# Performance work log

Measured on AMD Instinct MI355X. Metric: run time of the kernel, lower is better.

## Reference

```python
import jax, jax.numpy as jnp
import numpy as np

D_MODEL = 1024
NUM_HEADS = 16
D_FF = 4096
MAX_SEQ_LEN = 2048
THETA = 10000.0
EPS = 1e-5
B, S = 2, 2048


def setup_inputs() -> dict:
    key = jax.random.key(0)
    ks = jax.random.split(key, 10)
    scale = 0.02
    inp = {
        "in_features": jax.random.normal(ks[0], (B, S, D_MODEL), dtype=jnp.float32),
        "token_positions": jnp.broadcast_to(jnp.arange(S, dtype=jnp.int32), (B, S)),
        "q_w": jax.random.normal(ks[1], (D_MODEL, D_MODEL), dtype=jnp.float32) * scale,
        "k_w": jax.random.normal(ks[2], (D_MODEL, D_MODEL), dtype=jnp.float32) * scale,
        "v_w": jax.random.normal(ks[3], (D_MODEL, D_MODEL), dtype=jnp.float32) * scale,
        "o_w": jax.random.normal(ks[4], (D_MODEL, D_MODEL), dtype=jnp.float32) * scale,
        "ln1_w": jnp.ones((D_MODEL,), dtype=jnp.float32),
        "ln2_w": jnp.ones((D_MODEL,), dtype=jnp.float32),
        "ffn_w1": jax.random.normal(ks[5], (D_FF, D_MODEL), dtype=jnp.float32) * scale,
        "ffn_w2": jax.random.normal(ks[6], (D_MODEL, D_FF), dtype=jnp.float32) * scale,
        "ffn_w3": jax.random.normal(ks[7], (D_FF, D_MODEL), dtype=jnp.float32) * scale,
    }
    return inp


def _rmsnorm(x, w, eps=EPS):
    return x * jax.lax.rsqrt(jnp.mean(x * x, axis=-1, keepdims=True) + eps) * w


def _rope(x, pos, theta=THETA):
    # x: [B, H, S, Dh]; pos: [B, S] int
    dh = x.shape[-1]
    inv_freq = theta ** (-jnp.arange(0, dh, 2, dtype=jnp.float32) / dh)  # [Dh/2]
    ang = pos.astype(jnp.float32)[..., None] * inv_freq                  # [B, S, Dh/2]
    cos = jnp.cos(ang)[:, None, :, :]  # [B, 1, S, Dh/2]
    sin = jnp.sin(ang)[:, None, :, :]
    x1, x2 = x[..., 0::2], x[..., 1::2]
    r1 = x1 * cos - x2 * sin
    r2 = x1 * sin + x2 * cos
    return jnp.stack([r1, r2], axis=-1).reshape(x.shape)


def _block(x, pos, q_w, k_w, v_w, o_w, ln1_w, ln2_w, w1, w2, w3):
    b, s, d = x.shape
    h, dh = NUM_HEADS, d // NUM_HEADS
    # Pre-LN attention
    xn = _rmsnorm(x, ln1_w)
    q = jnp.einsum('bsd,ed->bse', xn, q_w).reshape(b, s, h, dh).transpose(0, 2, 1, 3)
    k = jnp.einsum('bsd,ed->bse', xn, k_w).reshape(b, s, h, dh).transpose(0, 2, 1, 3)
    v = jnp.einsum('bsd,ed->bse', xn, v_w).reshape(b, s, h, dh).transpose(0, 2, 1, 3)
    q = _rope(q, pos)
    k = _rope(k, pos)
    scores = jnp.einsum('bhqd,bhkd->bhqk', q, k) / jnp.sqrt(jnp.float32(dh))
    causal = jnp.tril(jnp.ones((s, s), dtype=bool))
    scores = jnp.where(causal, scores, jnp.float32(-1e9))
    attn = jax.nn.softmax(scores, axis=-1)
    ctx = jnp.einsum('bhqk,bhkd->bhqd', attn, v).transpose(0, 2, 1, 3).reshape(b, s, d)
    attn_out = jnp.einsum('bsd,ed->bse', ctx, o_w)
    x = x + attn_out
    # Pre-LN SwiGLU FFN
    xn2 = _rmsnorm(x, ln2_w)
    g = jnp.einsum('bsd,fd->bsf', xn2, w1)
    u = jnp.einsum('bsd,fd->bsf', xn2, w3)
    ffn_out = jnp.einsum('bsf,df->bsd', jax.nn.silu(g) * u, w2)
    return x + ffn_out


def reference(in_features, token_positions, q_w, k_w, v_w, o_w, ln1_w, ln2_w, ffn_w1, ffn_w2, ffn_w3):
    return _block(in_features, token_positions, q_w, k_w, v_w, o_w, ln1_w, ln2_w, ffn_w1, ffn_w2, ffn_w3)
```

## Files before the change

kernel.cpp:

```cpp
#include <hip/hip_runtime.h>
#include <hip/hip_bf16.h>

typedef __attribute__((ext_vector_type(8))) __bf16 bf16x8;
typedef __attribute__((ext_vector_type(4))) float f32x4;

#define DEV static __device__ __forceinline__

DEV unsigned short f2bf(float f) {
  __bf16 h = (__bf16)f;
  union { __bf16 h; unsigned short u; } v; v.h = h;
  return v.u;
}
DEV float bf2f(unsigned short h) {
  union { unsigned int u; float f; } v; v.u = ((unsigned int)h) << 16;
  return v.f;
}
DEV f32x4 mfma16(bf16x8 a, bf16x8 b, f32x4 c) {
  return __builtin_amdgcn_mfma_f32_16x16x32_bf16(a, b, c, 0, 0, 0);
}
DEV void gload_lds16(const void* g, void* l) {
  __builtin_amdgcn_global_load_lds((__attribute__((address_space(1))) void*)g,
                                   (__attribute__((address_space(3))) void*)l,
                                   16, 0, 0);
}
#if __has_builtin(__builtin_amdgcn_exp2f)
DEV float fexp2(float x) { return __builtin_amdgcn_exp2f(x); }
#else
DEV float fexp2(float x) { return exp2f(x); }
#endif

struct CvtArgs { const float* src[7]; int cum[8]; };
__global__ __launch_bounds__(256) void cvt_all(CvtArgs a, unsigned short* __restrict__ dst) {
  int i = (blockIdx.x * 256 + threadIdx.x) * 4;
  if (i >= a.cum[7]) return;
  int w = 0;
#pragma unroll 7
  for (int t = 0; t < 7; ++t) if (i >= a.cum[t + 1]) w = t + 1;
  float4 v = *(const float4*)(a.src[w] + (i - a.cum[w]));
  dst[i + 0] = f2bf(v.x);
  dst[i + 1] = f2bf(v.y);
  dst[i + 2] = f2bf(v.z);
  dst[i + 3] = f2bf(v.w);
}

__global__ __launch_bounds__(256) void rmsnorm_k(const float* __restrict__ x,
                                                 const float* __restrict__ w,
                                                 unsigned short* __restrict__ out) {
  int row = blockIdx.x;
  int tid = threadIdx.x;
  const float* xr = x + (size_t)row * 1024;
  float4 v = *(const float4*)(xr + tid * 4);
  float ss = v.x * v.x + v.y * v.y + v.z * v.z + v.w * v.w;
#pragma unroll
  for (int m = 32; m >= 1; m >>= 1) ss += __shfl_xor(ss, m);
  __shared__ float red[4];
  int wid = tid >> 6;
  if ((tid & 63) == 0) red[wid] = ss;
  __syncthreads();
  float tot = red[0] + red[1] + red[2] + red[3];
  float rs = rsqrtf(tot * (1.0f / 1024.0f) + 1e-5f);
  float4 wv = *(const float4*)(w + tid * 4);
  unsigned short* o = out + (size_t)row * 1024 + tid * 4;
  o[0] = f2bf(v.x * rs * wv.x);
  o[1] = f2bf(v.y * rs * wv.y);
  o[2] = f2bf(v.z * rs * wv.z);
  o[3] = f2bf(v.w * rs * wv.w);
}

__global__ __launch_bounds__(256) void rope2_k(unsigned short* __restrict__ q,
                                               unsigned short* __restrict__ k,
                                               const int* __restrict__ pos) {
  int gid = blockIdx.x * 256 + threadIdx.x;
  unsigned short* x = (gid < 2097152) ? q : k;
  int idx = gid & 2097151;
  int i = idx & 31;
  int s = (idx >> 5) & 2047;
  int bh = idx >> 16;
  int b = bh >> 4;
  float p = (float)pos[b * 2048 + s];
  float inv = exp2f(-(float)i * 0.4152410118609203f);
  float ang = p * inv;
  float sn = sinf(ang), cs = cosf(ang);
  size_t base = (((size_t)bh * 2048) + s) * 64 + 2 * i;
  float x1 = bf2f(x[base]), x2 = bf2f(x[base + 1]);
  x[base]     = f2bf(x1 * cs - x2 * sn);
  x[base + 1] = f2bf(x1 * sn + x2 * cs);
}

template <int MODE>
DEV void gemm8_body(const unsigned short* __restrict__ A, int lda,
                    const unsigned short* __restrict__ B, int ldb,
                    int bm, int bn, int kbase, int nt,
                    unsigned short* __restrict__ outb, float* __restrict__ outf,
                    const float* __restrict__ resid, const unsigned short* __restrict__ gate,
                    unsigned short* As, unsigned short* Bs) {
  const int tid = threadIdx.x;
  const int lane = tid & 63, wid = tid >> 6;
  const int wr = wid >> 2, wc = wid & 3;
  const int m0 = bm * 256, n0 = bn * 256;

  const int r0 = tid >> 2, r1 = 128 + (tid >> 2), cc = tid & 3;
  const int sc0 = (cc ^ ((r0 >> 1) & 3)) * 8;
  const int sc1 = (cc ^ ((r1 >> 1) & 3)) * 8;
  const size_t arow0 = (size_t)(m0 + r0) * lda, arow1 = (size_t)(m0 + r1) * lda;
  const size_t brow0 = (size_t)(n0 + r0) * ldb, brow1 = (size_t)(n0 + r1) * ldb;
  const int du0 = tid * 8, du1 = (512 + tid) * 8;

  auto stA = [&](int t, int kh) {
    unsigned short* d = As + ((((t & 1) << 1) | kh) * 8192);
    const unsigned short* s = A + kbase + t * 64 + kh * 32;
    gload_lds16(s + arow0 + sc0, d + du0);
    gload_lds16(s + arow1 + sc1, d + du1);
  };
  auto stB = [&](int t, int kh) {
    unsigned short* d = Bs + ((((t & 1) << 1) | kh) * 8192);
    const unsigned short* s = B + kbase + t * 64 + kh * 32;
    gload_lds16(s + brow0 + sc0, d + du0);
    gload_lds16(s + brow1 + sc1, d + du1);
  };

  const int fcol = ((lane >> 4) ^ ((lane >> 1) & 3)) * 8;
  const int frow = lane & 15;
  const int abase = (wr * 128 + frow) * 32 + fcol;
  const int bbase = (wc * 64 + frow) * 32 + fcol;

  f32x4 acc[8][4] = {};
  bf16x8 a[4], b[4];

#define LOADA(buf, ks, mh) { const unsigned short* p_ = As + (((buf) << 1) | (ks)) * 8192 + abase + (mh) * 2048; \
  a[0] = *(const bf16x8*)(p_); a[1] = *(const bf16x8*)(p_ + 512); \
  a[2] = *(const bf16x8*)(p_ + 1024); a[3] = *(const bf16x8*)(p_ + 1536); }
#define LOADB(buf, ks) { const unsigned short* p_ = Bs + (((buf) << 1) | (ks)) * 8192 + bbase; \
  b[0] = *(const bf16x8*)(p_); b[1] = *(const bf16x8*)(p_ + 512); \
  b[2] = *(const bf16x8*)(p_ + 1024); b[3] = *(const bf16x8*)(p_ + 1536); }
#define MFMAQ(mh) { _Pragma("unroll") for (int fi = 0; fi < 4; ++fi) \
  _Pragma("unroll") for (int j = 0; j < 4; ++j) \
    acc[(mh) * 4 + fi][j] = mfma16(a[fi], b[j], acc[(mh) * 4 + fi][j]); }
#define LGK0() { asm volatile("s_waitcnt lgkmcnt(0)" ::: "memory"); __builtin_amdgcn_sched_barrier(0); }

  stA(0, 0); stB(0, 0); stA(0, 1); stB(0, 1);
  stA(1, 0); stB(1, 0);
  asm volatile("s_waitcnt vmcnt(4)" ::: "memory");
  __builtin_amdgcn_s_barrier();

  for (int t = 0; t < nt; ++t) {
    const int buf = t & 1;
    LOADA(buf, 0, 0); LOADB(buf, 0);
    if (t + 1 < nt) stA(t + 1, 1);
    __builtin_amdgcn_s_barrier();
    LGK0();
    __builtin_amdgcn_s_setprio(1); MFMAQ(0); __builtin_amdgcn_s_setprio(0);
    __builtin_amdgcn_s_barrier();
    LOADA(buf, 0, 1);
    if (t + 1 < nt) stB(t + 1, 1);
    __builtin_amdgcn_s_barrier();
    LGK0();
    __builtin_amdgcn_s_setprio(1); MFMAQ(1); __builtin_amdgcn_s_setprio(0);
    __builtin_amdgcn_s_barrier();
    LOADA(buf, 1, 0); LOADB(buf, 1);
    if (t + 2 < nt) stA(t + 2, 0);
    __builtin_amdgcn_s_barrier();
    LGK0();
    __builtin_amdgcn_s_setprio(1); MFMAQ(0); __builtin_amdgcn_s_setprio(0);
    __builtin_amdgcn_s_barrier();
    LOADA(buf, 1, 1);
    if (t + 2 < nt) stB(t + 2, 0);
    __builtin_amdgcn_s_barrier();
    LGK0();
    __builtin_amdgcn_s_setprio(1); MFMAQ(1); __builtin_amdgcn_s_setprio(0);
    if (t + 1 < nt) {
      if (t + 2 < nt) { asm volatile("s_waitcnt vmcnt(4)" ::: "memory"); }
      else            { asm volatile("s_waitcnt vmcnt(0)" ::: "memory"); }
      __builtin_amdgcn_s_barrier();
    }
  }
#undef LOADA
#undef LOADB
#undef MFMAQ
#undef LGK0

#pragma unroll
  for (int i = 0; i < 8; ++i)
#pragma unroll
    for (int j = 0; j < 4; ++j)
#pragma unroll
      for (int r = 0; r < 4; ++r) {
        int m = m0 + wr * 128 + i * 16 + ((lane >> 4) << 2) + r;
        int n = n0 + wc * 64 + j * 16 + (lane & 15);
        float v = acc[i][j][r];
        if (MODE == 0) {
          unsigned short* dst = outb + ((n >= 1024) ? 4194304 : 0);
          int nn = n & 1023;
          int bb = m >> 11, s = m & 2047, hh = nn >> 6, dd = nn & 63;
          dst[(((size_t)bb * 16 + hh) * 2048 + s) * 64 + dd] = f2bf(v);
        } else if (MODE == 1) {
          int hh = m >> 6, dd = m & 63, bb = n >> 11, s = n & 2047;
          outb[(((size_t)bb * 16 + hh) * 64 + dd) * 2048 + s] = f2bf(v);
        } else if (MODE == 2) {
          size_t idx = (size_t)m * 1024 + n;
          outf[idx] = resid[idx] + v;
        } else if (MODE == 3) {
          outb[(size_t)m * 4096 + n] = f2bf(v);
        } else if (MODE == 4) {
          size_t idx = (size_t)m * 4096 + n;
          float g = bf2f(gate[idx]);
          outb[idx] = f2bf(g / (1.0f + __expf(-g)) * v);
        } else {
          outf[(size_t)m * 1024 + n] = v;
        }
      }
}

DEV void swz_map(int bid, int nwg, int MT, int& bm, int& bn) {
  int cpx = nwg >> 3;
  int sw = (bid & 7) * cpx + (bid >> 3);
  bm = sw % MT;
  bn = sw / MT;
}

template <int MODE>
__global__ __launch_bounds__(512, 2) void gemm8_k(const unsigned short* __restrict__ A, int lda,
                                                  const unsigned short* __restrict__ B, int ldb,
                                                  int MT, int kz, int nt,
                                                  unsigned short* __restrict__ outb,
                                                  float* __restrict__ outf,
                                                  const float* __restrict__ resid,
                                                  const unsigned short* __restrict__ gate) {
  __shared__ __align__(16) unsigned short lds[65536];
  int bm, bn;
  swz_map(blockIdx.x, gridDim.x, MT, bm, bn);
  int kb = kz * blockIdx.y;
  float* of = outf;
  if (MODE == 5) of += (size_t)blockIdx.y * 4194304;
  gemm8_body<MODE>(A, lda, B, ldb, bm, bn, kb, nt, outb, of, resid, gate, lds, lds + 32768);
}

__global__ __launch_bounds__(512, 2) void gemm8_qkv(const unsigned short* __restrict__ xn,
                                                    const unsigned short* __restrict__ wqk,
                                                    const unsigned short* __restrict__ wv,
                                                    unsigned short* __restrict__ qk_out,
                                                    unsigned short* __restrict__ vt_out) {
  __shared__ __align__(16) unsigned short lds[65536];
  int bid = blockIdx.x;
  if (bid < 128) {
    int bm, bn;
    swz_map(bid, 128, 16, bm, bn);
    gemm8_body<0>(xn, 1024, wqk, 1024, bm, bn, 0, 16, qk_out, nullptr, nullptr, nullptr, lds, lds + 32768);
  } else {
    bid -= 128;
    int bm, bn;
    swz_map(bid, 64, 4, bm, bn);
    gemm8_body<1>(wv, 1024, xn, 1024, bm, bn, 0, 16, vt_out, nullptr, nullptr, nullptr, lds, lds + 32768);
  }
}

__global__ __launch_bounds__(256) void gemm_wo(const unsigned short* __restrict__ A,
                                               const unsigned short* __restrict__ Bw,
                                               float* __restrict__ outf,
                                               const float* __restrict__ resid) {
  __shared__ __align__(16) unsigned short As[128 * 64];
  __shared__ __align__(16) unsigned short Bs[128 * 64];
  const int K = 1024, N = 1024;
  const int tid = threadIdx.x;
  const int wid = tid >> 6, lane = tid & 63;
  const int wr = wid >> 1, wc = wid & 1;
  const int m0 = blockIdx.x * 128, n0 = blockIdx.y * 128;
  const int sw = (lane & 7) * 8;
  f32x4 acc[4][4] = {};

  for (int k0 = 0; k0 < K; k0 += 64) {
    __syncthreads();
#pragma unroll
    for (int it = 0; it < 4; ++it) {
      int c = wid * 4 + it;
      int row = c * 8 + (lane >> 3);
      int col = ((lane & 7) ^ (row & 7)) * 8;
      gload_lds16(A + (size_t)(m0 + row) * K + k0 + col, As + c * 512);
      gload_lds16(Bw + (size_t)(n0 + row) * K + k0 + col, Bs + c * 512);
    }
    asm volatile("s_waitcnt vmcnt(0)" ::: "memory");
    __syncthreads();
#pragma unroll
    for (int kk = 0; kk < 2; ++kk) {
      const int kof = (kk * 32 + (lane >> 4) * 8) ^ sw;
      bf16x8 af[4], bfr[4];
#pragma unroll
      for (int i = 0; i < 4; ++i) {
        af[i]  = *(const bf16x8*)(As + (wr * 64 + i * 16 + (lane & 15)) * 64 + kof);
        bfr[i] = *(const bf16x8*)(Bs + (wc * 64 + i * 16 + (lane & 15)) * 64 + kof);
      }
#pragma unroll
      for (int i = 0; i < 4; ++i)
#pragma unroll
        for (int j = 0; j < 4; ++j) acc[i][j] = mfma16(af[i], bfr[j], acc[i][j]);
    }
  }
  const int rb = m0 + wr * 64 + ((lane >> 4) * 4);
  const int cb = n0 + wc * 64 + (lane & 15);
#pragma unroll
  for (int i = 0; i < 4; ++i)
#pragma unroll
    for (int r = 0; r < 4; ++r) {
      int m = rb + i * 16 + r;
#pragma unroll
      for (int j = 0; j < 4; ++j) {
        size_t idx = (size_t)m * N + cb + j * 16;
        outf[idx] = resid[idx] + acc[i][j][r];
      }
    }
}

__global__ __launch_bounds__(256) void reduce_k(float* __restrict__ out,
                                                const float* __restrict__ part) {
  int i = (blockIdx.x * 256 + threadIdx.x) * 4;
  float4 o = *(const float4*)(out + i);
  float4 p0 = *(const float4*)(part + i);
  float4 p1 = *(const float4*)(part + 4194304 + i);
  float4 p2 = *(const float4*)(part + 8388608 + i);
  float4 p3 = *(const float4*)(part + 12582912 + i);
  o.x += p0.x + p1.x + p2.x + p3.x;
  o.y += p0.y + p1.y + p2.y + p3.y;
  o.z += p0.z + p1.z + p2.z + p3.z;
  o.w += p0.w + p1.w + p2.w + p3.w;
  *(float4*)(out + i) = o;
}

__global__ __launch_bounds__(256) void attn_k(const unsigned short* __restrict__ q,
                                              const unsigned short* __restrict__ k,
                                              const unsigned short* __restrict__ vt,
                                              unsigned short* __restrict__ ctx) {
  __shared__ __align__(16) unsigned short Ks[2][64 * 64];
  __shared__ __align__(16) unsigned short Vs[2][64 * 64];
  __shared__ __align__(16) unsigned short Ps[4][16 * 64];
  const int bid = blockIdx.x;
  const int bh = (bid & 7) * 4 + ((bid >> 3) & 3);
  const int qt = 31 - (bid >> 5);
  const int tid = threadIdx.x, wid = tid >> 6, lane = tid & 63;
  const size_t bhS = (size_t)bh * 2048;
  const size_t bhD = (size_t)bh * 64 * 2048;
  const int b = bh >> 4, hh = bh & 15;
  const int sw = (lane & 7) * 8;
  const float SC2 = 0.18033688011112042f;

  const int c0 = wid * 2, c1 = wid * 2 + 1;
  const int row0 = c0 * 8 + (lane >> 3), row1 = c1 * 8 + (lane >> 3);
  const int col0 = ((lane & 7) ^ (row0 & 7)) * 8;
  const int col1 = ((lane & 7) ^ (row1 & 7)) * 8;

  auto stage = [&](int kt, int buf) {
    gload_lds16(k + (bhS + kt * 64 + row0) * 64 + col0, &Ks[buf][c0 * 512]);
    gload_lds16(k + (bhS + kt * 64 + row1) * 64 + col1, &Ks[buf][c1 * 512]);
    gload_lds16(vt + bhD + (size_t)row0 * 2048 + kt * 64 + col0, &Vs[buf][c0 * 512]);
    gload_lds16(vt + bhD + (size_t)row1 * 2048 + kt * 64 + col1, &Vs[buf][c1 * 512]);
  };

  const int q0 = qt * 64;
  bf16x8 qf[2];
  {
    const unsigned short* qp = q + (bhS + q0 + wid * 16 + (lane & 15)) * 64 + (lane >> 4) * 8;
    qf[0] = *(const bf16x8*)qp;
    qf[1] = *(const bf16x8*)(qp + 32);
#pragma unroll
    for (int jj = 0; jj < 8; ++jj) {
      qf[0][jj] = (__bf16)((float)qf[0][jj] * SC2);
      qf[1][jj] = (__bf16)((float)qf[1][jj] * SC2);
    }
  }
  float mrow[4], lrow[4];
  f32x4 o[4] = {};
#pragma unroll
  for (int r = 0; r < 4; ++r) { mrow[r] = -1e30f; lrow[r] = 0.0f; }
  const int rowb = q0 + wid * 16 + ((lane >> 4) * 4);

  stage(0, 0);
  if (qt > 0) { stage(1, 1); asm volatile("s_waitcnt vmcnt(4)" ::: "memory"); }
  else        {              asm volatile("s_waitcnt vmcnt(0)" ::: "memory"); }
  __builtin_amdgcn_s_barrier();

  for (int kt = 0; kt <= qt; ++kt) {
    const int cur = kt & 1;
    f32x4 s[4];
#pragma unroll
    for (int nt = 0; nt < 4; ++nt) {
      f32x4 z = {};
#pragma unroll
      for (int ks = 0; ks < 2; ++ks) {
        int kof = (ks * 32 + (lane >> 4) * 8) ^ sw;
        bf16x8 kf = *(const bf16x8*)(&Ks[cur][(nt * 16 + (lane & 15)) * 64 + kof]);
        z = mfma16(qf[ks], kf, z);
      }
      s[nt] = z;
    }
    const bool diag = (kt == qt);
    float pm[4];
    bool ok = true;
#pragma unroll
    for (int r = 0; r < 4; ++r) {
      float mx = -3e38f;
#pragma unroll
      for (int nt = 0; nt < 4; ++nt) {
        float val = s[nt][r];
        if (diag && (kt * 64 + nt * 16 + (lane & 15)) > (rowb + r)) val = -3e38f;
        s[nt][r] = val;
        mx = fmaxf(mx, val);
      }
      mx = fmaxf(mx, __shfl_xor(mx, 1));
      mx = fmaxf(mx, __shfl_xor(mx, 2));
      mx = fmaxf(mx, __shfl_xor(mx, 4));
      mx = fmaxf(mx, __shfl_xor(mx, 8));
      pm[r] = mx;
      ok = ok && (mx <= mrow[r] + 11.5f);
    }
    if (!__all(ok)) {
#pragma unroll
      for (int r = 0; r < 4; ++r) {
        float mn = fmaxf(mrow[r], pm[r]);
        float al = fexp2(mrow[r] - mn);
        lrow[r] *= al;
#pragma unroll
        for (int d = 0; d < 4; ++d) o[d][r] *= al;
        mrow[r] = mn;
      }
    }
#pragma unroll
    for (int r = 0; r < 4; ++r) {
      float sum = 0.0f;
#pragma unroll
      for (int nt = 0; nt < 4; ++nt) {
        float pv = fexp2(s[nt][r] - mrow[r]);
        s[nt][r] = pv;
        sum += pv;
      }
      lrow[r] += sum;
    }
#pragma unroll
    for (int nt = 0; nt < 4; ++nt)
#pragma unroll
      for (int r = 0; r < 4; ++r) {
        int qr = (lane >> 4) * 4 + r;
        Ps[wid][qr * 64 + ((nt * 16 + (lane & 15)) ^ ((qr & 7) * 8))] = f2bf(s[nt][r]);
      }
#pragma unroll
    for (int ks = 0; ks < 2; ++ks) {
      int qr2 = lane & 15;
      bf16x8 pf = *(const bf16x8*)(&Ps[wid][qr2 * 64 + ((ks * 32 + (lane >> 4) * 8) ^ ((qr2 & 7) * 8))]);
      int kof = (ks * 32 + (lane >> 4) * 8) ^ sw;
#pragma unroll
      for (int d = 0; d < 4; ++d) {
        bf16x8 vf = *(const bf16x8*)(&Vs[cur][(d * 16 + (lane & 15)) * 64 + kof]);
        o[d] = mfma16(pf, vf, o[d]);
      }
    }
    __builtin_amdgcn_s_barrier();
    if (kt + 2 <= qt) {
      stage(kt + 2, cur);
      asm volatile("s_waitcnt vmcnt(4)" ::: "memory");
    } else if (kt + 1 <= qt) {
      asm volatile("s_waitcnt vmcnt(0)" ::: "memory");
    }
    __builtin_amdgcn_s_barrier();
  }
#pragma unroll
  for (int r = 0; r < 4; ++r) {
    lrow[r] += __shfl_xor(lrow[r], 1);
    lrow[r] += __shfl_xor(lrow[r], 2);
    lrow[r] += __shfl_xor(lrow[r], 4);
    lrow[r] += __shfl_xor(lrow[r], 8);
  }
#pragma unroll
  for (int d = 0; d < 4; ++d)
#pragma unroll
    for (int r = 0; r < 4; ++r) {
      float val = o[d][r] / lrow[r];
      ctx[((size_t)b * 2048 + (rowb + r)) * 1024 + hh * 64 + d * 16 + (lane & 15)] = f2bf(val);
    }
}

extern "C" void kernel_launch(void* const* d_in, const int* in_sizes, int n_in,
                              void* d_out, int out_size, void* d_ws, size_t ws_size,
                              hipStream_t stream) {
  (void)in_sizes; (void)n_in; (void)out_size; (void)ws_size;
  const float* in_f = (const float*)d_in[0];
  const int* pos    = (const int*)d_in[1];
  const float* q_w  = (const float*)d_in[2];
  const float* k_w  = (const float*)d_in[3];
  const float* v_w  = (const float*)d_in[4];
  const float* o_w  = (const float*)d_in[5];
  const float* ln1  = (const float*)d_in[6];
  const float* ln2  = (const float*)d_in[7];
  const float* w1   = (const float*)d_in[8];
  const float* w2   = (const float*)d_in[9];
  const float* w3   = (const float*)d_in[10];
  float* out = (float*)d_out;

  unsigned short* ws = (unsigned short*)d_ws;
  unsigned short* wb   = ws;
  unsigned short* wqkb = wb;
  unsigned short* wvb  = wb + 2097152;
  unsigned short* wob  = wb + 3145728;
  unsigned short* w1b  = wb + 4194304;
  unsigned short* w2b  = wb + 8388608;
  unsigned short* w3b  = wb + 12582912;
  unsigned short* xn   = ws + 16777216;
  unsigned short* qb   = ws + 20971520;
  unsigned short* kb   = ws + 25165824;
  unsigned short* vb   = ws + 29360128;
  unsigned short* cx   = ws + 33554432;
  unsigned short* gb   = ws + 37748736;
  float* part          = (float*)(ws + 20971520);
  unsigned short* hb   = ws + 54525952;

  CvtArgs ca;
  ca.src[0] = q_w; ca.src[1] = k_w; ca.src[2] = v_w; ca.src[3] = o_w;
  ca.src[4] = w1;  ca.src[5] = w2;  ca.src[6] = w3;
  ca.cum[0] = 0;        ca.cum[1] = 1048576;  ca.cum[2] = 2097152;  ca.cum[3] = 3145728;
  ca.cum[4] = 4194304;  ca.cum[5] = 8388608;  ca.cum[6] = 12582912; ca.cum[7] = 16777216;
  cvt_all<<<16384, 256, 0, stream>>>(ca, wb);

  rmsnorm_k<<<4096, 256, 0, stream>>>(in_f, ln1, xn);

  gemm8_qkv<<<192, 512, 0, stream>>>(xn, wqkb, wvb, qb, vb);

  rope2_k<<<16384, 256, 0, stream>>>(qb, kb, pos);

  attn_k<<<1024, 256, 0, stream>>>(qb, kb, vb, cx);

  gemm_wo<<<dim3(32, 8), 256, 0, stream>>>(cx, wob, out, in_f);

  rmsnorm_k<<<4096, 256, 0, stream>>>(out, ln2, xn);

  gemm8_k<3><<<256, 512, 0, stream>>>(xn, 1024, w1b, 1024, 16, 0, 16, gb, nullptr, nullptr, nullptr);
  gemm8_k<4><<<256, 512, 0, stream>>>(xn, 1024, w3b, 1024, 16, 0, 16, hb, nullptr, nullptr, gb);
  gemm8_k<5><<<dim3(64, 4), 512, 0, stream>>>(hb, 4096, w2b, 4096, 16, 1024, 16, nullptr, part, nullptr, nullptr);

  reduce_k<<<4096, 256, 0, stream>>>(out, part);
}
```

Before: 294.4 us.

## Transpose attention scores, fuse rope q/k, fuse FFN down-proj with residual

The attention kernel now computes S^T (K as the A operand) so each lane owns one query row. Row max and sum then need only two cross-lane shuffles, and P is written to LDS as packed bf16 pairs with a padded stride instead of scalar swizzled stores. RoPE handles q and k in the same thread with half the grid. The split-K FFN down-projection plus separate reduce kernel is replaced by a templated 128x128 residual GEMM (K=4096) that adds into out directly. This removes the partial buffer traffic and one launch, but that GEMM loses the larger 256x256 tile and split-K parallelism. It also changes fexp2 to always use exp2f.

Measured after the change: 294.1 us. Within noise of the previous version (-0.1%).

```diff
diff --git a/kernel.cpp b/kernel.cpp
--- a/kernel.cpp
+++ b/kernel.cpp
@@ -15,6 +15,11 @@
   union { unsigned int u; float f; } v; v.u = ((unsigned int)h) << 16;
   return v.f;
 }
+DEV unsigned pkbf(float lo, float hi) {
+  union { __bf16 h[2]; unsigned u; } v;
+  v.h[0] = (__bf16)lo; v.h[1] = (__bf16)hi;
+  return v.u;
+}
 DEV f32x4 mfma16(bf16x8 a, bf16x8 b, f32x4 c) {
   return __builtin_amdgcn_mfma_f32_16x16x32_bf16(a, b, c, 0, 0, 0);
 }
@@ -23,11 +28,7 @@
                                    (__attribute__((address_space(3))) void*)l,
                                    16, 0, 0);
 }
-#if __has_builtin(__builtin_amdgcn_exp2f)
-DEV float fexp2(float x) { return __builtin_amdgcn_exp2f(x); }
-#else
 DEV float fexp2(float x) { return exp2f(x); }
-#endif
 
 struct CvtArgs { const float* src[7]; int cum[8]; };
 __global__ __launch_bounds__(256) void cvt_all(CvtArgs a, unsigned short* __restrict__ dst) {
@@ -70,9 +71,7 @@
 __global__ __launch_bounds__(256) void rope2_k(unsigned short* __restrict__ q,
                                                unsigned short* __restrict__ k,
                                                const int* __restrict__ pos) {
-  int gid = blockIdx.x * 256 + threadIdx.x;
-  unsigned short* x = (gid < 2097152) ? q : k;
-  int idx = gid & 2097151;
+  int idx = blockIdx.x * 256 + threadIdx.x;
   int i = idx & 31;
   int s = (idx >> 5) & 2047;
   int bh = idx >> 16;
@@ -82,9 +81,12 @@
   float ang = p * inv;
   float sn = sinf(ang), cs = cosf(ang);
   size_t base = (((size_t)bh * 2048) + s) * 64 + 2 * i;
-  float x1 = bf2f(x[base]), x2 = bf2f(x[base + 1]);
-  x[base]     = f2bf(x1 * cs - x2 * sn);
-  x[base + 1] = f2bf(x1 * sn + x2 * cs);
+  float q1 = bf2f(q[base]), q2 = bf2f(q[base + 1]);
+  q[base]     = f2bf(q1 * cs - q2 * sn);
+  q[base + 1] = f2bf(q1 * sn + q2 * cs);
+  float k1 = bf2f(k[base]), k2 = bf2f(k[base + 1]);
+  k[base]     = f2bf(k1 * cs - k2 * sn);
+  k[base + 1] = f2bf(k1 * sn + k2 * cs);
 }
 
 template <int MODE>
@@ -201,12 +203,10 @@
           outf[idx] = resid[idx] + v;
         } else if (MODE == 3) {
           outb[(size_t)m * 4096 + n] = f2bf(v);
-        } else if (MODE == 4) {
+        } else {
           size_t idx = (size_t)m * 4096 + n;
           float g = bf2f(gate[idx]);
           outb[idx] = f2bf(g / (1.0f + __expf(-g)) * v);
-        } else {
-          outf[(size_t)m * 1024 + n] = v;
         }
       }
 }
@@ -221,7 +221,7 @@
 template <int MODE>
 __global__ __launch_bounds__(512, 2) void gemm8_k(const unsigned short* __restrict__ A, int lda,
                                                   const unsigned short* __restrict__ B, int ldb,
-                                                  int MT, int kz, int nt,
+                                                  int MT, int nt,
                                                   unsigned short* __restrict__ outb,
                                                   float* __restrict__ outf,
                                                   const float* __restrict__ resid,
@@ -229,10 +229,7 @@
   __shared__ __align__(16) unsigned short lds[65536];
   int bm, bn;
   swz_map(blockIdx.x, gridDim.x, MT, bm, bn);
-  int kb = kz * blockIdx.y;
-  float* of = outf;
-  if (MODE == 5) of += (size_t)blockIdx.y * 4194304;
-  gemm8_body<MODE>(A, lda, B, ldb, bm, bn, kb, nt, outb, of, resid, gate, lds, lds + 32768);
+  gemm8_body<MODE>(A, lda, B, ldb, bm, bn, 0, nt, outb, outf, resid, gate, lds, lds + 32768);
 }
 
 __global__ __launch_bounds__(512, 2) void gemm8_qkv(const unsigned short* __restrict__ xn,
@@ -254,13 +251,14 @@
   }
 }
 
-__global__ __launch_bounds__(256) void gemm_wo(const unsigned short* __restrict__ A,
-                                               const unsigned short* __restrict__ Bw,
-                                               float* __restrict__ outf,
-                                               const float* __restrict__ resid) {
+template <int K>
+__global__ __launch_bounds__(256) void gemm_res(const unsigned short* __restrict__ A,
+                                                const unsigned short* __restrict__ Bw,
+                                                float* __restrict__ outf,
+                                                const float* __restrict__ resid) {
   __shared__ __align__(16) unsigned short As[128 * 64];
   __shared__ __align__(16) unsigned short Bs[128 * 64];
-  const int K = 1024, N = 1024;
+  const int N = 1024;
   const int tid = threadIdx.x;
   const int wid = tid >> 6, lane = tid & 63;
   const int wr = wid >> 1, wc = wid & 1;
@@ -310,28 +308,13 @@
     }
 }
 
-__global__ __launch_bounds__(256) void reduce_k(float* __restrict__ out,
-                                                const float* __restrict__ part) {
-  int i = (blockIdx.x * 256 + threadIdx.x) * 4;
-  float4 o = *(const float4*)(out + i);
-  float4 p0 = *(const float4*)(part + i);
-  float4 p1 = *(const float4*)(part + 4194304 + i);
-  float4 p2 = *(const float4*)(part + 8388608 + i);
-  float4 p3 = *(const float4*)(part + 12582912 + i);
-  o.x += p0.x + p1.x + p2.x + p3.x;
-  o.y += p0.y + p1.y + p2.y + p3.y;
-  o.z += p0.z + p1.z + p2.z + p3.z;
-  o.w += p0.w + p1.w + p2.w + p3.w;
-  *(float4*)(out + i) = o;
-}
-
 __global__ __launch_bounds__(256) void attn_k(const unsigned short* __restrict__ q,
                                               const unsigned short* __restrict__ k,
                                               const unsigned short* __restrict__ vt,
                                               unsigned short* __restrict__ ctx) {
-  __shared__ __align__(16) unsigned short Ks[2][64 * 64];
-  __shared__ __align__(16) unsigned short Vs[2][64 * 64];
-  __shared__ __align__(16) unsigned short Ps[4][16 * 64];
+  __shared__ __align__(16) unsigned short Ks[2][4096];
+  __shared__ __align__(16) unsigned short Vs[2][4096];
+  __shared__ __align__(16) unsigned short Ps[4][16 * 72];
   const int bid = blockIdx.x;
   const int bh = (bid & 7) * 4 + ((bid >> 3) & 3);
   const int qt = 31 - (bid >> 5);
@@ -340,6 +323,7 @@
   const size_t bhD = (size_t)bh * 64 * 2048;
   const int b = bh >> 4, hh = bh & 15;
   const int sw = (lane & 7) * 8;
+  const int h4 = lane >> 4, l15 = lane & 15;
   const float SC2 = 0.18033688011112042f;
 
   const int c0 = wid * 2, c1 = wid * 2 + 1;
@@ -357,7 +341,7 @@
   const int q0 = qt * 64;
   bf16x8 qf[2];
   {
-    const unsigned short* qp = q + (bhS + q0 + wid * 16 + (lane & 15)) * 64 + (lane >> 4) * 8;
+    const unsigned short* qp = q + (bhS + q0 + wid * 16 + l15) * 64 + h4 * 8;
     qf[0] = *(const bf16x8*)qp;
     qf[1] = *(const bf16x8*)(qp + 32);
 #pragma unroll
@@ -366,11 +350,10 @@
       qf[1][jj] = (__bf16)((float)qf[1][jj] * SC2);
     }
   }
-  float mrow[4], lrow[4];
+  float mrow = -1e30f, lrow = 0.0f;
   f32x4 o[4] = {};
-#pragma unroll
-  for (int r = 0; r < 4; ++r) { mrow[r] = -1e30f; lrow[r] = 0.0f; }
-  const int rowb = q0 + wid * 16 + ((lane >> 4) * 4);
+  const int qg = q0 + wid * 16 + l15;
+  const int rowb = q0 + wid * 16 + (h4 << 2);
 
   stage(0, 0);
   if (qt > 0) { stage(1, 1); asm volatile("s_waitcnt vmcnt(4)" ::: "memory"); }
@@ -379,75 +362,66 @@
 
   for (int kt = 0; kt <= qt; ++kt) {
     const int cur = kt & 1;
-    f32x4 s[4];
+    float s[16];
 #pragma unroll
     for (int nt = 0; nt < 4; ++nt) {
       f32x4 z = {};
 #pragma unroll
       for (int ks = 0; ks < 2; ++ks) {
-        int kof = (ks * 32 + (lane >> 4) * 8) ^ sw;
-        bf16x8 kf = *(const bf16x8*)(&Ks[cur][(nt * 16 + (lane & 15)) * 64 + kof]);
-        z = mfma16(qf[ks], kf, z);
-      }
-      s[nt] = z;
-    }
-    const bool diag = (kt == qt);
-    float pm[4];
-    bool ok = true;
-#pragma unroll
-    for (int r = 0; r < 4; ++r) {
-      float mx = -3e38f;
+        int kof = (ks * 32 + h4 * 8) ^ sw;
+        bf16x8 kf = *(const bf16x8*)(&Ks[cur][(nt * 16 + l15) * 64 + kof]);
+        z = mfma16(kf, qf[ks], z);
+      }
+      s[nt * 4 + 0] = z[0]; s[nt * 4 + 1] = z[1];
+      s[nt * 4 + 2] = z[2]; s[nt * 4 + 3] = z[3];
+    }
+    if (kt == qt) {
+#pragma unroll
+      for (int nt = 0; nt < 4; ++nt)
+#pragma unroll
+        for (int r = 0; r < 4; ++r) {
+          int key = q0 + nt * 16 + (h4 << 2) + r;
+          if (key > qg) s[nt * 4 + r] = -3e38f;
+        }
+    }
+    float pmax = s[0];
+#pragma unroll
+    for (int i = 1; i < 16; ++i) pmax = fmaxf(pmax, s[i]);
+    pmax = fmaxf(pmax, __shfl_xor(pmax, 16));
+    pmax = fmaxf(pmax, __shfl_xor(pmax, 32));
+    if (!__all(pmax <= mrow + 11.5f)) {
+      float mnew = fmaxf(mrow, pmax);
+      float dl = mrow - mnew;
+      mrow = mnew;
+      lrow *= fexp2(dl);
+#pragma unroll
+      for (int r = 0; r < 4; ++r) {
+        float ar = fexp2(__shfl(dl, (h4 << 2) + r, 16));
+#pragma unroll
+        for (int d = 0; d < 4; ++d) o[d][r] *= ar;
+      }
+    }
+    float sum = 0.0f;
+#pragma unroll
+    for (int i = 0; i < 16; ++i) { s[i] = fexp2(s[i] - mrow); sum += s[i]; }
+    lrow += sum;
+    {
+      unsigned short* pr = &Ps[wid][l15 * 72 + (h4 << 2)];
 #pragma unroll
       for (int nt = 0; nt < 4; ++nt) {
-        float val = s[nt][r];
-        if (diag && (kt * 64 + nt * 16 + (lane & 15)) > (rowb + r)) val = -3e38f;
-        s[nt][r] = val;
-        mx = fmaxf(mx, val);
-      }
-      mx = fmaxf(mx, __shfl_xor(mx, 1));
-      mx = fmaxf(mx, __shfl_xor(mx, 2));
-      mx = fmaxf(mx, __shfl_xor(mx, 4));
-      mx = fmaxf(mx, __shfl_xor(mx, 8));
-      pm[r] = mx;
-      ok = ok && (mx <= mrow[r] + 11.5f);
-    }
-    if (!__all(ok)) {
-#pragma unroll
-      for (int r = 0; r < 4; ++r) {
-        float mn = fmaxf(mrow[r], pm[r]);
-        float al = fexp2(mrow[r] - mn);
-        lrow[r] *= al;
-#pragma unroll
-        for (int d = 0; d < 4; ++d) o[d][r] *= al;
-        mrow[r] = mn;
-      }
-    }
-#pragma unroll
-    for (int r = 0; r < 4; ++r) {
-      float sum = 0.0f;
-#pragma unroll
-      for (int nt = 0; nt < 4; ++nt) {
-        float pv = fexp2(s[nt][r] - mrow[r]);
-        s[nt][r] = pv;
-        sum += pv;
-      }
-      lrow[r] += sum;
-    }
-#pragma unroll
-    for (int nt = 0; nt < 4; ++nt)
-#pragma unroll
-      for (int r = 0; r < 4; ++r) {
-        int qr = (lane >> 4) * 4 + r;
-        Ps[wid][qr * 64 + ((nt * 16 + (lane & 15)) ^ ((qr & 7) * 8))] = f2bf(s[nt][r]);
-      }
+        uint2 w;
+        w.x = pkbf(s[4 * nt], s[4 * nt + 1]);
+        w.y = pkbf(s[4 * nt + 2], s[4 * nt + 3]);
+        *(uint2*)(pr + nt * 16) = w;
+      }
+    }
 #pragma unroll
     for (int ks = 0; ks < 2; ++ks) {
-      int qr2 = lane & 15;
-      bf16x8 pf = *(const bf16x8*)(&Ps[wid][qr2 * 64 + ((ks * 32 + (lane >> 4) * 8) ^ ((qr2 & 7) * 8))]);
-      int kof = (ks * 32 + (lane >> 4) * 8) ^ sw;
+      bf16x8 pf = *(const bf16x8*)(&Ps[wid][l15 * 72 + ks * 32 + (h4 << 3)]);
+      int kof = (ks * 32 + h4 * 8) ^ sw;
 #pragma unroll
       for (int d = 0; d < 4; ++d) {
-        bf16x8 vf = *(const bf16x8*)(&Vs[cur][(d * 16 + (lane & 15)) * 64 + kof]);
+        bf16x8 vf = *(const bf16x8*)(&Vs[cur][(d * 16 + l15) * 64 + kof]);
         o[d] = mfma16(pf, vf, o[d]);
       }
     }
@@ -460,20 +434,16 @@
     }
     __builtin_amdgcn_s_barrier();
   }
+  lrow += __shfl_xor(lrow, 16);
+  lrow += __shfl_xor(lrow, 32);
+  float inv = 1.0f / lrow;
 #pragma unroll
   for (int r = 0; r < 4; ++r) {
-    lrow[r] += __shfl_xor(lrow[r], 1);
-    lrow[r] += __shfl_xor(lrow[r], 2);
-    lrow[r] += __shfl_xor(lrow[r], 4);
-    lrow[r] += __shfl_xor(lrow[r], 8);
+    float invr = __shfl(inv, (h4 << 2) + r, 16);
+#pragma unroll
+    for (int d = 0; d < 4; ++d)
+      ctx[((size_t)b * 2048 + (rowb + r)) * 1024 + hh * 64 + d * 16 + l15] = f2bf(o[d][r] * invr);
   }
-#pragma unroll
-  for (int d = 0; d < 4; ++d)
-#pragma unroll
-    for (int r = 0; r < 4; ++r) {
-      float val = o[d][r] / lrow[r];
-      ctx[((size_t)b * 2048 + (rowb + r)) * 1024 + hh * 64 + d * 16 + (lane & 15)] = f2bf(val);
-    }
 }
 
 extern "C" void kernel_launch(void* const* d_in, const int* in_sizes, int n_in,
@@ -507,7 +477,6 @@
   unsigned short* vb   = ws + 29360128;
   unsigned short* cx   = ws + 33554432;
   unsigned short* gb   = ws + 37748736;
-  float* part          = (float*)(ws + 20971520);
   unsigned short* hb   = ws + 54525952;
 
   CvtArgs ca;
@@ -521,17 +490,16 @@
 
   gemm8_qkv<<<192, 512, 0, stream>>>(xn, wqkb, wvb, qb, vb);
 
-  rope2_k<<<16384, 256, 0, stream>>>(qb, kb, pos);
+  rope2_k<<<8192, 256, 0, stream>>>(qb, kb, pos);
 
   attn_k<<<1024, 256, 0, stream>>>(qb, kb, vb, cx);
 
-  gemm_wo<<<dim3(32, 8), 256, 0, stream>>>(cx, wob, out, in_f);
+  gemm_res<1024><<<dim3(32, 8), 256, 0, stream>>>(cx, wob, out, in_f);
 
   rmsnorm_k<<<4096, 256, 0, stream>>>(out, ln2, xn);
 
-  gemm8_k<3><<<256, 512, 0, stream>>>(xn, 1024, w1b, 1024, 16, 0, 16, gb, nullptr, nullptr, nullptr);
-  gemm8_k<4><<<256, 512, 0, stream>>>(xn, 1024, w3b, 1024, 16, 0, 16, hb, nullptr, nullptr, gb);
-  gemm8_k<5><<<dim3(64, 4), 512, 0, stream>>>(hb, 4096, w2b, 4096, 16, 1024, 16, nullptr, part, nullptr, nullptr);
-
-  reduce_k<<<4096, 256, 0, stream>>>(out, part);
-}
+  gemm8_k<3><<<256, 512, 0, stream>>>(xn, 1024, w1b, 1024, 16, 16, gb, nullptr, nullptr, nullptr);
+  gemm8_k<4><<<256, 512, 0, stream>>>(xn, 1024, w3b, 1024, 16, 16, hb, nullptr, nullptr, gb);
+
+  gemm_res<4096><<<dim3(32, 8), 256, 0, stream>>>(hb, w2b, out, out);
+}
```
